# Optimization experiments

Hardware: AMD Instinct MI355X
Metric: run time of the kernel (lower is better)

Reference implementation:

```python
import jax, jax.numpy as jnp
import numpy as np

NUM_ENTS = 80000
NUM_WORDS = 20000
N_NODES = NUM_ENTS + NUM_WORDS  # 100000
H = 200          # args.n_hidden
NB = 100         # args.n_bases -> block-diagonal blocks
SUB = H // NB    # 2x2 blocks
NREL = 16        # num_static_rels * 2 (forward + inverse relations)
E = 300000       # edges in the static graph
RRELU_SLOPE = (1.0 / 8.0 + 1.0 / 3.0) / 2.0  # eval-mode rrelu = leaky relu with mean slope


def setup_inputs() -> dict:
    key = jax.random.key(0)
    k0, k1, k2, k3, k4, k5 = jax.random.split(key, 6)
    # nn.init.normal_ on dynamic_emb
    dynamic_emb = jax.random.normal(k0, (NUM_ENTS, H), dtype=jnp.float32)
    # xavier_normal_ on words_emb
    xav = float(np.sqrt(2.0 / (NUM_WORDS + H)))
    words_emb = jax.random.normal(k1, (NUM_WORDS, H), dtype=jnp.float32) * xav
    # RGCN block-diagonal weights: (num_rels, n_bases, submat_in, submat_out)
    weight = jax.random.normal(k2, (NREL, NB, SUB, SUB), dtype=jnp.float32) * float(1.0 / np.sqrt(SUB))
    src = jax.random.randint(k3, (E,), 0, N_NODES)
    dst = jax.random.randint(k4, (E,), 0, N_NODES)
    etype = jax.random.randint(k5, (E,), 0, NREL)
    return {"dynamic_emb": dynamic_emb, "words_emb": words_emb, "weight": weight,
            "src": src, "dst": dst, "etype": etype}


def reference(dynamic_emb, words_emb, weight, src, dst, etype):
    # ndata['h'] = cat(dynamic_emb, words_emb)
    h = jnp.concatenate([dynamic_emb, words_emb], axis=0)          # (N, H)
    # msg_func: per-edge block-diagonal transform of source features
    hs = h[src].reshape(E, NB, SUB)                                # gather src feats
    W = weight[etype]                                              # (E, NB, SUB, SUB) per-edge blocks
    msg = jnp.einsum('ebi,ebio->ebo', hs, W).reshape(E, H)         # block matmul
    # fn.sum aggregation into destination nodes
    agg = jax.ops.segment_sum(msg, dst, num_segments=N_NODES)      # (N, H)
    # apply_func: multiply by node norm = 1/in-degree (0 for isolated nodes)
    indeg = jax.ops.segment_sum(jnp.ones((E,), jnp.float32), dst, num_segments=N_NODES)
    norm = jnp.where(indeg > 0, 1.0 / jnp.maximum(indeg, 1.0), 0.0)
    hn = agg * norm[:, None]
    # activation F.rrelu (eval mode -> deterministic mean slope); dropout inactive at eval
    act = jnp.where(hn >= 0, hn, hn * RRELU_SLOPE)
    # slice entity rows and L2-normalize (layer_norm=True path)
    static_emb = act[:NUM_ENTS]
    nrm = jnp.linalg.norm(static_emb, axis=1, keepdims=True)
    out = static_emb / jnp.maximum(nrm, 1e-12)
    # original returns (self.h, static_emb): the same tensor twice
    return (out, out)
```

## Files before the change

### kernel.cpp

```cpp
#include <hip/hip_runtime.h>

#define NUM_ENTS   80000
#define NUM_WORDS  20000
#define N_NODES    100000
#define H          200
#define NB         100
#define NREL       16
#define E_EDGES    300000
#define SLOTS      32
#define RRELU_SLOPE 0.22916666666666666f

typedef float v4f __attribute__((ext_vector_type(4)));

__global__ void build_lists_kernel(const int* __restrict__ src,
                                   const int* __restrict__ dst,
                                   const int* __restrict__ etype,
                                   int* __restrict__ counts,
                                   int* __restrict__ slots) {
    int e = blockIdx.x * blockDim.x + threadIdx.x;
    if (e >= E_EDGES) return;
    int d = dst[e];
    if (d >= NUM_ENTS) return;
    int pos = atomicAdd(&counts[d], 1);
    if (pos < SLOTS)
        slots[d * SLOTS + pos] = src[e] | (etype[e] << 17);
}

__global__ void gather_finalize_kernel(const float* __restrict__ dyn,
                                       const float* __restrict__ words,
                                       const float* __restrict__ weight,
                                       const int* __restrict__ counts,
                                       const int* __restrict__ slots,
                                       float* __restrict__ out) {
    int wave = threadIdx.x >> 6;
    int lane = threadIdx.x & 63;
    int node = blockIdx.x * 4 + wave;
    if (node >= NUM_ENTS) return;

    int deg = counts[node];
    int n = deg < SLOTS ? deg : SLOTS;

    const int* sl = slots + node * SLOTS;
    int slotv = sl[lane & 31];

    const bool act = (lane < 50);

    float a0 = 0.f, a1 = 0.f, a2 = 0.f, a3 = 0.f;

    #pragma unroll
    for (int j = 0; j < 4; ++j) {
        int packed = __shfl(slotv, j);
        if (j >= n) packed = 0;
        float m = (j < n) ? 1.f : 0.f;
        int s  = packed & 0x1FFFF;
        int et = packed >> 17;
        const float* hrow = (s < NUM_ENTS) ? (dyn + s * H)
                                           : (words + (s - NUM_ENTS) * H);
        const float* wrel = weight + et * (NB * 4);
        if (act) {
            v4f hv = *(const v4f*)(hrow + 4 * lane);
            v4f w0 = *(const v4f*)(wrel + 8 * lane);
            v4f w1 = *(const v4f*)(wrel + 8 * lane + 4);
            a0 += m * (hv.x * w0.x + hv.y * w0.z);
            a1 += m * (hv.x * w0.y + hv.y * w0.w);
            a2 += m * (hv.z * w1.x + hv.w * w1.z);
            a3 += m * (hv.z * w1.y + hv.w * w1.w);
        }
    }
    for (int j = 4; j < n; ++j) {
        int packed = __shfl(slotv, j);
        int s  = packed & 0x1FFFF;
        int et = packed >> 17;
        const float* hrow = (s < NUM_ENTS) ? (dyn + s * H)
                                           : (words + (s - NUM_ENTS) * H);
        const float* wrel = weight + et * (NB * 4);
        if (act) {
            v4f hv = *(const v4f*)(hrow + 4 * lane);
            v4f w0 = *(const v4f*)(wrel + 8 * lane);
            v4f w1 = *(const v4f*)(wrel + 8 * lane + 4);
            a0 += hv.x * w0.x + hv.y * w0.z;
            a1 += hv.x * w0.y + hv.y * w0.w;
            a2 += hv.z * w1.x + hv.w * w1.z;
            a3 += hv.z * w1.y + hv.w * w1.w;
        }
    }

    float nrm = deg > 0 ? 1.f / (float)deg : 0.f;
    a0 *= nrm; a1 *= nrm; a2 *= nrm; a3 *= nrm;
    a0 = (a0 >= 0.f) ? a0 : a0 * RRELU_SLOPE;
    a1 = (a1 >= 0.f) ? a1 : a1 * RRELU_SLOPE;
    a2 = (a2 >= 0.f) ? a2 : a2 * RRELU_SLOPE;
    a3 = (a3 >= 0.f) ? a3 : a3 * RRELU_SLOPE;

    float ss = a0 * a0 + a1 * a1 + a2 * a2 + a3 * a3;
    #pragma unroll
    for (int off = 32; off >= 1; off >>= 1)
        ss += __shfl_xor(ss, off, 64);
    float inv = 1.f / fmaxf(sqrtf(ss), 1e-12f);

    if (act) {
        v4f r;
        r.x = a0 * inv; r.y = a1 * inv; r.z = a2 * inv; r.w = a3 * inv;
        float* o0 = out + node * H + 4 * lane;
        float* o1 = o0 + NUM_ENTS * H;
        __builtin_nontemporal_store(r, (v4f*)o0);
        __builtin_nontemporal_store(r, (v4f*)o1);
    }
}

extern "C" void kernel_launch(void* const* d_in, const int* in_sizes, int n_in,
                              void* d_out, int out_size, void* d_ws, size_t ws_size,
                              hipStream_t stream) {
    const float* dyn    = (const float*)d_in[0];
    const float* words  = (const float*)d_in[1];
    const float* weight = (const float*)d_in[2];
    const int*   src    = (const int*)d_in[3];
    const int*   dst    = (const int*)d_in[4];
    const int*   etype  = (const int*)d_in[5];
    float* out = (float*)d_out;

    int* counts = (int*)d_ws;
    int* slots  = counts + NUM_ENTS;

    hipMemsetAsync(counts, 0, (size_t)NUM_ENTS * sizeof(int), stream);

    build_lists_kernel<<<(E_EDGES + 255) / 256, 256, 0, stream>>>(
        src, dst, etype, counts, slots);

    gather_finalize_kernel<<<(NUM_ENTS + 3) / 4, 256, 0, stream>>>(
        dyn, words, weight, counts, slots, out);
}
```

Before: 259.0 us.

## Stage relation weights in LDS and front-load first four row gathers

Each block now copies the full 16-relation block-diagonal weight table into shared memory and reads per-edge weights from LDS instead of global memory. Blocks grow to 8 waves (512 threads) and the first up-to-four source-row loads are issued together before any arithmetic to raise memory-level parallelism. The degree is made wave-uniform with readfirstlane. The cost is a 25.6 KB LDS fill plus a barrier in every block, which may limit occupancy and adds redundant global reads per block.

```diff
diff --git a/kernel.cpp b/kernel.cpp
--- a/kernel.cpp
+++ b/kernel.cpp
@@ -9,6 +9,7 @@
 #define E_EDGES    300000
 #define SLOTS      32
 #define RRELU_SLOPE 0.22916666666666666f
+#define WFLOATS    (NREL * NB * 4)
 
 typedef float v4f __attribute__((ext_vector_type(4)));
 
@@ -32,58 +33,85 @@
                                        const int* __restrict__ counts,
                                        const int* __restrict__ slots,
                                        float* __restrict__ out) {
+    __shared__ float wlds[WFLOATS];
+
     int wave = threadIdx.x >> 6;
     int lane = threadIdx.x & 63;
-    int node = blockIdx.x * 4 + wave;
-    if (node >= NUM_ENTS) return;
+    int node = blockIdx.x * 8 + wave;
 
-    int deg = counts[node];
+    int deg = __builtin_amdgcn_readfirstlane(counts[node]);
     int n = deg < SLOTS ? deg : SLOTS;
+    int slotv = slots[node * SLOTS + (lane & 31)];
 
-    const int* sl = slots + node * SLOTS;
-    int slotv = sl[lane & 31];
+    {
+        const v4f* wg = (const v4f*)weight;
+        v4f* wl = (v4f*)wlds;
+        #pragma unroll
+        for (int i = 0; i < 4; ++i) {
+            int idx = (int)threadIdx.x + i * 512;
+            if (idx < WFLOATS / 4) wl[idx] = wg[idx];
+        }
+    }
+    __syncthreads();
 
     const bool act = (lane < 50);
 
+    int p0 = __shfl(slotv, 0);
+    int p1 = __shfl(slotv, 1);
+    int p2 = __shfl(slotv, 2);
+    int p3 = __shfl(slotv, 3);
+
+    v4f h0 = {0.f,0.f,0.f,0.f}, h1 = {0.f,0.f,0.f,0.f};
+    v4f h2 = {0.f,0.f,0.f,0.f}, h3 = {0.f,0.f,0.f,0.f};
+
+    int n4 = n < 4 ? n : 4;
+    if (act) {
+        switch (n4) {
+        case 4: { int s = p3 & 0x1FFFF;
+                  const float* r = (s < NUM_ENTS) ? dyn + s * H : words + (s - NUM_ENTS) * H;
+                  h3 = *(const v4f*)(r + 4 * lane); } [[fallthrough]];
+        case 3: { int s = p2 & 0x1FFFF;
+                  const float* r = (s < NUM_ENTS) ? dyn + s * H : words + (s - NUM_ENTS) * H;
+                  h2 = *(const v4f*)(r + 4 * lane); } [[fallthrough]];
+        case 2: { int s = p1 & 0x1FFFF;
+                  const float* r = (s < NUM_ENTS) ? dyn + s * H : words + (s - NUM_ENTS) * H;
+                  h1 = *(const v4f*)(r + 4 * lane); } [[fallthrough]];
+        case 1: { int s = p0 & 0x1FFFF;
+                  const float* r = (s < NUM_ENTS) ? dyn + s * H : words + (s - NUM_ENTS) * H;
+                  h0 = *(const v4f*)(r + 4 * lane); } [[fallthrough]];
+        default: break;
+        }
+    }
+
     float a0 = 0.f, a1 = 0.f, a2 = 0.f, a3 = 0.f;
 
-    #pragma unroll
-    for (int j = 0; j < 4; ++j) {
-        int packed = __shfl(slotv, j);
-        if (j >= n) packed = 0;
-        float m = (j < n) ? 1.f : 0.f;
-        int s  = packed & 0x1FFFF;
-        int et = packed >> 17;
-        const float* hrow = (s < NUM_ENTS) ? (dyn + s * H)
-                                           : (words + (s - NUM_ENTS) * H);
-        const float* wrel = weight + et * (NB * 4);
-        if (act) {
-            v4f hv = *(const v4f*)(hrow + 4 * lane);
-            v4f w0 = *(const v4f*)(wrel + 8 * lane);
-            v4f w1 = *(const v4f*)(wrel + 8 * lane + 4);
-            a0 += m * (hv.x * w0.x + hv.y * w0.z);
-            a1 += m * (hv.x * w0.y + hv.y * w0.w);
-            a2 += m * (hv.z * w1.x + hv.w * w1.z);
-            a3 += m * (hv.z * w1.y + hv.w * w1.w);
-        }
+#define WACC(HV, P) {                                                    \
+        int et = ((P) >> 17) & 15;                                       \
+        const float* wl = wlds + et * (NB * 4) + 8 * lane;               \
+        v4f w0 = *(const v4f*)wl;                                        \
+        v4f w1 = *(const v4f*)(wl + 4);                                  \
+        a0 += HV.x * w0.x + HV.y * w0.z;                                 \
+        a1 += HV.x * w0.y + HV.y * w0.w;                                 \
+        a2 += HV.z * w1.x + HV.w * w1.z;                                 \
+        a3 += HV.z * w1.y + HV.w * w1.w;                                 \
     }
+    if (act) {
+        WACC(h0, p0)
+        WACC(h1, p1)
+        WACC(h2, p2)
+        WACC(h3, p3)
+    }
+
     for (int j = 4; j < n; ++j) {
         int packed = __shfl(slotv, j);
         int s  = packed & 0x1FFFF;
-        int et = packed >> 17;
-        const float* hrow = (s < NUM_ENTS) ? (dyn + s * H)
-                                           : (words + (s - NUM_ENTS) * H);
-        const float* wrel = weight + et * (NB * 4);
+        const float* r = (s < NUM_ENTS) ? dyn + s * H : words + (s - NUM_ENTS) * H;
         if (act) {
-            v4f hv = *(const v4f*)(hrow + 4 * lane);
-            v4f w0 = *(const v4f*)(wrel + 8 * lane);
-            v4f w1 = *(const v4f*)(wrel + 8 * lane + 4);
-            a0 += hv.x * w0.x + hv.y * w0.z;
-            a1 += hv.x * w0.y + hv.y * w0.w;
-            a2 += hv.z * w1.x + hv.w * w1.z;
-            a3 += hv.z * w1.y + hv.w * w1.w;
+            v4f hv = *(const v4f*)(r + 4 * lane);
+            WACC(hv, packed)
         }
     }
+#undef WACC
 
     float nrm = deg > 0 ? 1.f / (float)deg : 0.f;
     a0 *= nrm; a1 *= nrm; a2 *= nrm; a3 *= nrm;
@@ -99,12 +127,12 @@
     float inv = 1.f / fmaxf(sqrtf(ss), 1e-12f);
 
     if (act) {
-        v4f r;
-        r.x = a0 * inv; r.y = a1 * inv; r.z = a2 * inv; r.w = a3 * inv;
+        v4f rr;
+        rr.x = a0 * inv; rr.y = a1 * inv; rr.z = a2 * inv; rr.w = a3 * inv;
         float* o0 = out + node * H + 4 * lane;
         float* o1 = o0 + NUM_ENTS * H;
-        __builtin_nontemporal_store(r, (v4f*)o0);
-        __builtin_nontemporal_store(r, (v4f*)o1);
+        __builtin_nontemporal_store(rr, (v4f*)o0);
+        __builtin_nontemporal_store(rr, (v4f*)o1);
     }
 }
 
@@ -127,6 +155,6 @@
     build_lists_kernel<<<(E_EDGES + 255) / 256, 256, 0, stream>>>(
         src, dst, etype, counts, slots);
 
-    gather_finalize_kernel<<<(NUM_ENTS + 3) / 4, 256, 0, stream>>>(
+    gather_finalize_kernel<<<NUM_ENTS / 8, 512, 0, stream>>>(
         dyn, words, weight, counts, slots, out);
 }
```

Result: no change. 256.2 us (-1.1%).
